# Kernel optimization log

Measured on AMD Instinct MI355X. Metric: run time of the kernel, lower is better.

Reference implementation:

```python
import jax, jax.numpy as jnp
import numpy as np

N_NODES = 50000
N_EDGES = 800000
N_GRAPHS = 512
D_IN, D_HID, D_EMB = 64, 128, 128


def _lin_params(key, d_in, d_out):
    kw, kb = jax.random.split(key)
    scale = 1.0 / np.sqrt(d_in)
    W = jax.random.uniform(kw, (d_in, d_out), minval=-scale, maxval=scale, dtype=jnp.float32)
    b = jax.random.uniform(kb, (d_out,), minval=-scale, maxval=scale, dtype=jnp.float32)
    return W, b


def setup_inputs() -> dict:
    key = jax.random.key(0)
    ks = jax.random.split(key, 12)
    x = jax.random.normal(ks[0], (N_NODES, D_IN), dtype=jnp.float32)
    edge_index = jax.random.randint(ks[1], (2, N_EDGES), 0, N_NODES, dtype=jnp.int64)
    batch = jnp.sort(jax.random.randint(ks[2], (N_NODES,), 0, N_GRAPHS, dtype=jnp.int64))
    Wq1, bq1 = _lin_params(ks[3], D_IN, D_HID)
    Wk1, bk1 = _lin_params(ks[4], D_IN, D_HID)
    Wv1, bv1 = _lin_params(ks[5], D_IN, D_HID)
    Ws1, bs1 = _lin_params(ks[6], D_IN, D_HID)
    Wq2, bq2 = _lin_params(ks[7], D_HID, D_EMB)
    Wk2, bk2 = _lin_params(ks[8], D_HID, D_EMB)
    Wv2, bv2 = _lin_params(ks[9], D_HID, D_EMB)
    Ws2, bs2 = _lin_params(ks[10], D_HID, D_EMB)
    return {
        'x': x, 'edge_index': edge_index, 'batch': batch,
        'Wq1': Wq1, 'bq1': bq1, 'Wk1': Wk1, 'bk1': bk1, 'Wv1': Wv1, 'bv1': bv1, 'Ws1': Ws1, 'bs1': bs1,
        'Wq2': Wq2, 'bq2': bq2, 'Wk2': Wk2, 'bk2': bk2, 'Wv2': Wv2, 'bv2': bv2, 'Ws2': Ws2, 'bs2': bs2,
    }


def _transformer_conv(x, src, dst, Wq, bq, Wk, bk, Wv, bv, Ws, bs):
    # PyG TransformerConv, heads=1, concat=True, root_weight=True, no edge_attr.
    d = Wq.shape[1]
    q = x @ Wq + bq          # [N, d]
    k = x @ Wk + bk
    v = x @ Wv + bv
    # per-edge attention score (gather at src/dst)
    score = jnp.sum(q[dst] * k[src], axis=-1) / jnp.sqrt(jnp.float32(d))  # [E]
    # segment softmax over destination neighborhoods
    m = jax.ops.segment_max(score, dst, num_segments=N_NODES)
    e = jnp.exp(score - m[dst])
    s = jax.ops.segment_sum(e, dst, num_segments=N_NODES)
    alpha = e / (s[dst] + 1e-16)  # [E]
    out = jax.ops.segment_sum(alpha[:, None] * v[src], dst, num_segments=N_NODES)  # [N, d]
    return out + (x @ Ws + bs)  # skip connection


def reference(x, edge_index, batch,
              Wq1, bq1, Wk1, bk1, Wv1, bv1, Ws1, bs1,
              Wq2, bq2, Wk2, bk2, Wv2, bv2, Ws2, bs2):
    src, dst = edge_index[0], edge_index[1]
    h = _transformer_conv(x, src, dst, Wq1, bq1, Wk1, bk1, Wv1, bv1, Ws1, bs1)
    h = jax.nn.relu(h)
    h = _transformer_conv(h, src, dst, Wq2, bq2, Wk2, bk2, Wv2, bv2, Ws2, bs2)
    # global mean pool over batch index
    sums = jax.ops.segment_sum(h, batch, num_segments=N_GRAPHS)
    counts = jax.ops.segment_sum(jnp.ones((h.shape[0],), dtype=h.dtype), batch, num_segments=N_GRAPHS)
    return sums / jnp.maximum(counts, 1.0)[:, None]
```

## Files before the change

kernel.cpp:

```cpp
#include <hip/hip_runtime.h>
#include <hip/hip_fp8.h>
#include <math.h>


constexpr int D1 = 64;
constexpr int DH = 128;
constexpr int SCHUNK = 1024;
constexpr float QSCALE2 = 0.12751743f;

typedef __attribute__((ext_vector_type(8))) short short8v;
typedef __attribute__((ext_vector_type(4))) float f32x4;
typedef __attribute__((ext_vector_type(2))) float f32x2;

#if __has_builtin(__builtin_amdgcn_cvt_pk_f32_fp8)
#define HW_FP8_DEC 1
#endif

__device__ inline unsigned short bf16r(float f) {
  unsigned u = __float_as_uint(f);
  return (unsigned short)((u + 0x7fffu + ((u >> 16) & 1u)) >> 16);
}

__device__ inline unsigned pack_bf16_2(float a, float b) {
  return (unsigned)bf16r(a) | ((unsigned)bf16r(b) << 16);
}

__device__ inline float bf16f(unsigned short u) {
  return __uint_as_float(((unsigned)u) << 16);
}

__device__ inline unsigned char fp8e(float f) {
  __hip_fp8_e4m3 h(f);
  return h.__x;
}

#ifndef HW_FP8_DEC
__device__ inline float fp8f_sw(unsigned b) {
  unsigned e = (b >> 3) & 15u, mm = b & 7u;
  float v;
  if (e == 0) v = (float)mm * 0.001953125f;
  else v = __uint_as_float(((e + 119u) << 23) | (mm << 20));
  return (b & 0x80u) ? -v : v;
}
#endif

__device__ inline void fp8_dec8(unsigned lo, unsigned hi, float* w) {
#ifdef HW_FP8_DEC
  f32x2 p01 = __builtin_amdgcn_cvt_pk_f32_fp8((int)lo, false);
  f32x2 p23 = __builtin_amdgcn_cvt_pk_f32_fp8((int)lo, true);
  f32x2 p45 = __builtin_amdgcn_cvt_pk_f32_fp8((int)hi, false);
  f32x2 p67 = __builtin_amdgcn_cvt_pk_f32_fp8((int)hi, true);
  w[0] = p01[0]; w[1] = p01[1]; w[2] = p23[0]; w[3] = p23[1];
  w[4] = p45[0]; w[5] = p45[1]; w[6] = p67[0]; w[7] = p67[1];
#else
  w[0] = fp8f_sw(lo & 0xffu); w[1] = fp8f_sw((lo >> 8) & 0xffu);
  w[2] = fp8f_sw((lo >> 16) & 0xffu); w[3] = fp8f_sw(lo >> 24);
  w[4] = fp8f_sw(hi & 0xffu); w[5] = fp8f_sw((hi >> 8) & 0xffu);
  w[6] = fp8f_sw((hi >> 16) & 0xffu); w[7] = fp8f_sw(hi >> 24);
#endif
}


__global__ __launch_bounds__(256) void hist_prep(
    const int* __restrict__ dst, int* __restrict__ deg, int* __restrict__ rank,
    int E, int nbHist,
    const float* w0, const float* w1, const float* w2, const float* w3,
    const float* w4, const float* w5, const float* w6, const float* w7,
    unsigned short* t0, unsigned short* t1, unsigned short* t2,
    unsigned short* t3, unsigned short* t4, unsigned short* t5,
    unsigned short* t6, unsigned short* t7,
    const float4* __restrict__ x, uint2* __restrict__ xb, int n4) {
  int b = blockIdx.x;
  int tid = threadIdx.x;
  if (b < nbHist) {
    int i = b * 256 + tid;
    if (i < (E >> 2)) {
      int4 d4 = ((const int4*)dst)[i];
      int4 r4;
      r4.x = atomicAdd(&deg[d4.x], 1);
      r4.y = atomicAdd(&deg[d4.y], 1);
      r4.z = atomicAdd(&deg[d4.z], 1);
      r4.w = atomicAdd(&deg[d4.w], 1);
      ((int4*)rank)[i] = r4;
    }
    if (b == 0 && tid == 0) {
      for (int e = E & ~3; e < E; ++e) rank[e] = atomicAdd(&deg[dst[e]], 1);
    }
    return;
  }
  int g = b - nbHist;
  if (g < 512) {
    int m = g >> 6, bx = g & 63;
    const float* W;
    unsigned short* T;
    switch (m) {
      case 0: W = w0; T = t0; break;
      case 1: W = w1; T = t1; break;
      case 2: W = w2; T = t2; break;
      case 3: W = w3; T = t3; break;
      case 4: W = w4; T = t4; break;
      case 5: W = w5; T = t5; break;
      case 6: W = w6; T = t6; break;
      default: W = w7; T = t7; break;
    }
    int din = (m < 4) ? 64 : 128;
    int total = din * 128;
    int i = bx * 256 + tid;
    if (i < total) {
      int r = i >> 7, c = i & 127;
      T[c * din + r] = bf16r(W[i]);
    }
    return;
  }
  int bx = g - 512;
  for (int i = bx * 256 + tid; i < n4; i += 256 * 256) {
    float4 v = x[i];
    uint2 o;
    o.x = pack_bf16_2(v.x, v.y);
    o.y = pack_bf16_2(v.z, v.w);
    xb[i] = o;
  }
}


__global__ void scan_chunks(const int* __restrict__ deg, int* __restrict__ incl,
                            int* __restrict__ sums, int N) {
  __shared__ int lds[256];
  int b = blockIdx.x, tid = threadIdx.x;
  int base = b * SCHUNK + tid * 4;
  int e0 = (base + 0 < N) ? deg[base + 0] : 0;
  int e1 = (base + 1 < N) ? deg[base + 1] : 0;
  int e2 = (base + 2 < N) ? deg[base + 2] : 0;
  int e3 = (base + 3 < N) ? deg[base + 3] : 0;
  int t0 = e0, t1 = t0 + e1, t2 = t1 + e2, t3 = t2 + e3;
  lds[tid] = t3;
  __syncthreads();
  for (int off = 1; off < 256; off <<= 1) {
    int v = (tid >= off) ? lds[tid - off] : 0;
    __syncthreads();
    lds[tid] += v;
    __syncthreads();
  }
  int excl = (tid > 0) ? lds[tid - 1] : 0;
  if (base + 0 < N) incl[base + 0] = t0 + excl;
  if (base + 1 < N) incl[base + 1] = t1 + excl;
  if (base + 2 < N) incl[base + 2] = t2 + excl;
  if (base + 3 < N) incl[base + 3] = t3 + excl;
  if (tid == 255) sums[b] = lds[255];
}

__global__ void finalize_rowptr(const int* __restrict__ incl, const int* __restrict__ sums,
                                int* __restrict__ rowptr, int N) {
  int n = blockIdx.x * blockDim.x + threadIdx.x;
  if (n < N) {
    int ch = n / SCHUNK;
    int off = 0;
    for (int i = 0; i < ch; ++i) off += sums[i];
    rowptr[n + 1] = incl[n] + off;
  }
  if (n == 0) rowptr[0] = 0;
}


template <int DIN>
__device__ __forceinline__ void gemm4_tile(
    int bx, int y, int tid,
    const unsigned short* __restrict__ xb, int N,
    const unsigned short* __restrict__ Wt0, const float* __restrict__ B0,
    const unsigned short* __restrict__ Wt1, const float* __restrict__ B1,
    const unsigned short* __restrict__ Wt2, const float* __restrict__ B2,
    const unsigned short* __restrict__ Wt3, const float* __restrict__ B3,
    unsigned short* __restrict__ Qb, unsigned char* __restrict__ KV,
    unsigned short* __restrict__ Os) {
  constexpr int DS = DIN + 8;
  __shared__ __align__(16) unsigned short As[128 * DS];
  __shared__ __align__(16) unsigned short Bs[128 * DS];
  const unsigned short* Wt;
  const float* Bias;
  switch (y) {
    case 0: Wt = Wt0; Bias = B0; break;
    case 1: Wt = Wt1; Bias = B1; break;
    case 2: Wt = Wt2; Bias = B2; break;
    default: Wt = Wt3; Bias = B3; break;
  }
  int n0 = bx * 128;

  constexpr int CPR = DIN / 8;
  constexpr int ACH = 128 * CPR;
#pragma unroll
  for (int c = tid; c < ACH; c += 512) {
    int row = c / CPR, c8 = c - row * CPR;
    int n = n0 + row;
    uint4 val = {0u, 0u, 0u, 0u};
    if (n < N) val = *(const uint4*)&xb[(size_t)n * DIN + c8 * 8];
    *(uint4*)&As[row * DS + c8 * 8] = val;
  }
#pragma unroll
  for (int c = tid; c < ACH; c += 512) {
    int row = c / CPR, c8 = c - row * CPR;
    uint4 val = *(const uint4*)&Wt[(size_t)row * DIN + c8 * 8];
    *(uint4*)&Bs[row * DS + c8 * 8] = val;
  }
  __syncthreads();

  int w = tid >> 6, lane = tid & 63, lr = lane & 15, lg = lane >> 4;
  int wr = w >> 2;
  int wc = w & 3;
  constexpr int KS = DIN / 32;

  short8v a[4][KS];
#pragma unroll
  for (int af = 0; af < 4; ++af)
#pragma unroll
    for (int ks = 0; ks < KS; ++ks)
      a[af][ks] = *(const short8v*)&As[(wr * 64 + af * 16 + lr) * DS + ks * 32 + lg * 8];

  f32x4 acc[4][2];
#pragma unroll
  for (int af = 0; af < 4; ++af)
#pragma unroll
    for (int nf = 0; nf < 2; ++nf) acc[af][nf] = (f32x4){0.f, 0.f, 0.f, 0.f};

#pragma unroll
  for (int ks = 0; ks < KS; ++ks) {
#pragma unroll
    for (int nf = 0; nf < 2; ++nf) {
      short8v b = *(const short8v*)&Bs[(wc * 32 + nf * 16 + lr) * DS + ks * 32 + lg * 8];
#pragma unroll
      for (int af = 0; af < 4; ++af)
        acc[af][nf] = __builtin_amdgcn_mfma_f32_16x16x32_bf16(a[af][ks], b, acc[af][nf], 0, 0, 0);
    }
  }

#pragma unroll
  for (int af = 0; af < 4; ++af) {
    int rbase = n0 + wr * 64 + af * 16 + lg * 4;
#pragma unroll
    for (int nf = 0; nf < 2; ++nf) {
      int col = wc * 32 + nf * 16 + lr;
      float bias = Bias[col];
      if (y == 0) {
#pragma unroll
        for (int r = 0; r < 4; ++r) {
          int n = rbase + r;
          if (n < N) Qb[(size_t)n * 128 + col] = bf16r((acc[af][nf][r] + bias) * QSCALE2);
        }
      } else if (y == 1) {
#pragma unroll
        for (int r = 0; r < 4; ++r) {
          int n = rbase + r;
          if (n < N) KV[(size_t)n * 256 + col] = fp8e(acc[af][nf][r] + bias);
        }
      } else if (y == 2) {
#pragma unroll
        for (int r = 0; r < 4; ++r) {
          int n = rbase + r;
          if (n < N) KV[(size_t)n * 256 + 128 + col] = fp8e(acc[af][nf][r] + bias);
        }
      } else {
#pragma unroll
        for (int r = 0; r < 4; ++r) {
          int n = rbase + r;
          if (n < N) Os[(size_t)n * 128 + col] = bf16r(acc[af][nf][r] + bias);
        }
      }
    }
  }
}


template <int DIN>
__global__ __launch_bounds__(512) void fill_gemm1(
    const int* __restrict__ src, const int* __restrict__ dst,
    const int* __restrict__ rank, const int* __restrict__ rowptr,
    int* __restrict__ csr_src, int E, int epb4,
    const unsigned short* __restrict__ xb, int N,
    const unsigned short* __restrict__ Wt0, const float* __restrict__ B0,
    const unsigned short* __restrict__ Wt1, const float* __restrict__ B1,
    const unsigned short* __restrict__ Wt2, const float* __restrict__ B2,
    const unsigned short* __restrict__ Wt3, const float* __restrict__ B3,
    unsigned short* __restrict__ Qb, unsigned char* __restrict__ KV,
    unsigned short* __restrict__ Os) {
  int b = blockIdx.x;
  int b5 = b / 5, r5 = b - b5 * 5;
  if (r5 == 0) {
    int e4 = E >> 2;
    int end = min((b5 + 1) * epb4, e4);
    for (int i = b5 * epb4 + threadIdx.x; i < end; i += 512) {
      int4 d4 = ((const int4*)dst)[i];
      int4 r4 = ((const int4*)rank)[i];
      int4 s4 = ((const int4*)src)[i];
      csr_src[rowptr[d4.x] + r4.x] = s4.x;
      csr_src[rowptr[d4.y] + r4.y] = s4.y;
      csr_src[rowptr[d4.z] + r4.z] = s4.z;
      csr_src[rowptr[d4.w] + r4.w] = s4.w;
    }
    if (b5 == 0 && threadIdx.x == 0) {
      for (int e = E & ~3; e < E; ++e) csr_src[rowptr[dst[e]] + rank[e]] = src[e];
    }
    return;
  }
  int g = b5 * 4 + r5 - 1;
  gemm4_tile<DIN>(g >> 2, g & 3, threadIdx.x, xb, N, Wt0, B0, Wt1, B1,
                  Wt2, B2, Wt3, B3, Qb, KV, Os);
}

template <int DIN>
__global__ __launch_bounds__(512) void gemm4(
    const unsigned short* __restrict__ xb, int N,
    const unsigned short* __restrict__ Wt0, const float* __restrict__ B0,
    const unsigned short* __restrict__ Wt1, const float* __restrict__ B1,
    const unsigned short* __restrict__ Wt2, const float* __restrict__ B2,
    const unsigned short* __restrict__ Wt3, const float* __restrict__ B3,
    unsigned short* __restrict__ Qb, unsigned char* __restrict__ KV,
    unsigned short* __restrict__ Os) {
  gemm4_tile<DIN>(blockIdx.x, blockIdx.y, threadIdx.x, xb, N, Wt0, B0, Wt1, B1,
                  Wt2, B2, Wt3, B3, Qb, KV, Os);
}


template <bool RELU>
__global__ __launch_bounds__(256) void edge_agg4(
    const unsigned short* __restrict__ qb, const unsigned char* __restrict__ kv,
    const int* __restrict__ rowptr, const int* __restrict__ csr_src,
    const unsigned short* __restrict__ skipb, unsigned short* __restrict__ outp,
    int N) {
  int tid = threadIdx.x;
  int lane = tid & 63;
  int wv = tid >> 6;
  int n = blockIdx.x * 4 + wv;
  if (n >= N) return;
  int g4 = lane >> 4;
  int sl = lane & 15;
  uint4 qp = *(const uint4*)&qb[(size_t)n * 128 + 8 * sl];
  float q0 = bf16f((unsigned short)(qp.x & 0xffff)), q1 = bf16f((unsigned short)(qp.x >> 16));
  float q2 = bf16f((unsigned short)(qp.y & 0xffff)), q3 = bf16f((unsigned short)(qp.y >> 16));
  float q4 = bf16f((unsigned short)(qp.z & 0xffff)), q5 = bf16f((unsigned short)(qp.z >> 16));
  float q6 = bf16f((unsigned short)(qp.w & 0xffff)), q7 = bf16f((unsigned short)(qp.w >> 16));
  int beg = rowptr[n];
  int deg = rowptr[n + 1] - beg;
  float m = -1e30f, lsum = 0.f;
  float acc[8];
#pragma unroll
  for (int j = 0; j < 8; ++j) acc[j] = 0.f;
  int cnt = (deg - g4 + 3) >> 2;
  if (cnt < 0) cnt = 0;
  const int* cp = csr_src + beg + g4;
  unsigned ko = 8u * sl, vo = 128u + 8u * sl;
  uint2 k0 = {0, 0}, k1 = {0, 0};
  uint2 v0 = {0, 0}, v1 = {0, 0};
  if (cnt >= 1) {
    unsigned r = (unsigned)cp[0] * 256u;
    k0 = *(const uint2*)(kv + r + ko);
    v0 = *(const uint2*)(kv + r + vo);
  }
  if (cnt >= 2) {
    unsigned r = (unsigned)cp[4] * 256u;
    k1 = *(const uint2*)(kv + r + ko);
    v1 = *(const uint2*)(kv + r + vo);
  }
  for (int it = 0; it < cnt; ++it) {
    uint2 kc = k0;
    uint2 vc = v0;
    k0 = k1;
    v0 = v1;
    if (it + 2 < cnt) {
      unsigned r = (unsigned)cp[4 * (it + 2)] * 256u;
      k1 = *(const uint2*)(kv + r + ko);
      v1 = *(const uint2*)(kv + r + vo);
    }
    float kd[8];
    fp8_dec8(kc.x, kc.y, kd);
    float d = q0 * kd[0] + q1 * kd[1] + q2 * kd[2] + q3 * kd[3] +
              q4 * kd[4] + q5 * kd[5] + q6 * kd[6] + q7 * kd[7];
#pragma unroll
    for (int off = 1; off < 16; off <<= 1) d += __shfl_xor(d, off);
    float w[8];
    fp8_dec8(vc.x, vc.y, w);
    if (d > m + 8.f) {
      float cf = exp2f(m - d);
      lsum = lsum * cf + 1.f;
#pragma unroll
      for (int j = 0; j < 8; ++j) acc[j] = acc[j] * cf + w[j];
      m = d;
    } else {
      float ef = exp2f(d - m);
      lsum += ef;
#pragma unroll
      for (int j = 0; j < 8; ++j) acc[j] += ef * w[j];
    }
  }
#pragma unroll
  for (int ofs = 16; ofs <= 32; ofs <<= 1) {
    float mo = __shfl_xor(m, ofs);
    float lo = __shfl_xor(lsum, ofs);
    float ao[8];
#pragma unroll
    for (int j = 0; j < 8; ++j) ao[j] = __shfl_xor(acc[j], ofs);
    float M = fmaxf(m, mo);
    float c1 = exp2f(m - M);
    float c2 = exp2f(mo - M);
    lsum = lsum * c1 + lo * c2;
#pragma unroll
    for (int j = 0; j < 8; ++j) acc[j] = acc[j] * c1 + ao[j] * c2;
    m = M;
  }
  if (lane < 16) {
    float rl = (deg > 0) ? 1.f / (lsum + 1e-16f) : 0.f;
    uint4 sp = *(const uint4*)&skipb[(size_t)n * 128 + 8 * sl];
    float o0 = bf16f((unsigned short)(sp.x & 0xffff)) + acc[0] * rl;
    float o1 = bf16f((unsigned short)(sp.x >> 16)) + acc[1] * rl;
    float o2 = bf16f((unsigned short)(sp.y & 0xffff)) + acc[2] * rl;
    float o3 = bf16f((unsigned short)(sp.y >> 16)) + acc[3] * rl;
    float o4 = bf16f((unsigned short)(sp.z & 0xffff)) + acc[4] * rl;
    float o5 = bf16f((unsigned short)(sp.z >> 16)) + acc[5] * rl;
    float o6 = bf16f((unsigned short)(sp.w & 0xffff)) + acc[6] * rl;
    float o7 = bf16f((unsigned short)(sp.w >> 16)) + acc[7] * rl;
    if (RELU) {
      o0 = fmaxf(o0, 0.f); o1 = fmaxf(o1, 0.f); o2 = fmaxf(o2, 0.f); o3 = fmaxf(o3, 0.f);
      o4 = fmaxf(o4, 0.f); o5 = fmaxf(o5, 0.f); o6 = fmaxf(o6, 0.f); o7 = fmaxf(o7, 0.f);
    }
    uint4 pk;
    pk.x = pack_bf16_2(o0, o1);
    pk.y = pack_bf16_2(o2, o3);
    pk.z = pack_bf16_2(o4, o5);
    pk.w = pack_bf16_2(o6, o7);
    *(uint4*)&outp[(size_t)n * 128 + 8 * sl] = pk;
  }
}


__global__ __launch_bounds__(128) void pool_kernel(const unsigned short* __restrict__ h,
                                                   const int* __restrict__ batch,
                                                   float* __restrict__ out, int N) {
  int g = blockIdx.x;
  int lo = 0, hi = N;
  while (lo < hi) { int mid = (lo + hi) >> 1; if (batch[mid] < g) lo = mid + 1; else hi = mid; }
  int s0 = lo;
  hi = N;
  while (lo < hi) { int mid = (lo + hi) >> 1; if (batch[mid] <= g) lo = mid + 1; else hi = mid; }
  int s1 = lo;
  int j = threadIdx.x;
  float acc = 0.f;
  for (int n = s0; n < s1; ++n) acc += bf16f(h[(size_t)n * 128 + j]);
  out[(size_t)g * 128 + j] = acc / fmaxf((float)(s1 - s0), 1.f);
}


extern "C" void kernel_launch(void* const* d_in, const int* in_sizes, int n_in,
                              void* d_out, int out_size, void* d_ws, size_t ws_size,
                              hipStream_t stream) {
  const float* x = (const float*)d_in[0];
  const int* ei = (const int*)d_in[1];
  const int* batch = (const int*)d_in[2];
  const float* Wq1 = (const float*)d_in[3];
  const float* bq1 = (const float*)d_in[4];
  const float* Wk1 = (const float*)d_in[5];
  const float* bk1 = (const float*)d_in[6];
  const float* Wv1 = (const float*)d_in[7];
  const float* bv1 = (const float*)d_in[8];
  const float* Ws1 = (const float*)d_in[9];
  const float* bs1 = (const float*)d_in[10];
  const float* Wq2 = (const float*)d_in[11];
  const float* bq2 = (const float*)d_in[12];
  const float* Wk2 = (const float*)d_in[13];
  const float* bk2 = (const float*)d_in[14];
  const float* Wv2 = (const float*)d_in[15];
  const float* bv2 = (const float*)d_in[16];
  const float* Ws2 = (const float*)d_in[17];
  const float* bs2 = (const float*)d_in[18];

  int N = in_sizes[0] / D1;
  int E = in_sizes[1] / 2;
  int NG = out_size / DH;
  const int* src = ei;
  const int* dst = ei + E;

  char* ws = (char*)d_ws;
  unsigned short* qb = (unsigned short*)ws;  ws += (size_t)N * DH * 2;
  unsigned char* kvb = (unsigned char*)ws;   ws += (size_t)N * 256;
  ws = (char*)(((size_t)ws + 255) & ~(size_t)255);
  unsigned short* sb = (unsigned short*)ws;  ws += (size_t)N * DH * 2;
  unsigned short* h1b = (unsigned short*)ws; ws += (size_t)N * DH * 2;
  unsigned short* xb = (unsigned short*)ws;  ws += (size_t)N * D1 * 2;
  unsigned short* wt[8];
  for (int m = 0; m < 8; ++m) {
    int din = (m < 4) ? 64 : 128;
    wt[m] = (unsigned short*)ws;
    ws += (size_t)128 * din * 2;
  }
  ws = (char*)(((size_t)ws + 255) & ~(size_t)255);
  int* rowptr = (int*)ws; ws += (size_t)(N + 1) * 4;
  ws = (char*)(((size_t)ws + 255) & ~(size_t)255);
  int* deg = (int*)ws;  ws += (size_t)N * 4;
  int* incl = (int*)ws; ws += (size_t)N * 4;
  int* sums = (int*)ws; ws += 1024;
  int* rank = (int*)ws; ws += (size_t)E * 4;
  int* csr = (int*)ws;  ws += (size_t)E * 4;

  int nch = (N + SCHUNK - 1) / SCHUNK;
  int nbHist = ((E >> 2) + 255) / 256;
  int nb = (N + 127) / 128;
  int epb4 = ((E >> 2) + nb - 1) / nb;

  hipMemsetAsync(deg, 0, (size_t)N * 4, stream);

  hist_prep<<<nbHist + 768, 256, 0, stream>>>(
      dst, deg, rank, E, nbHist, Wq1, Wk1, Wv1, Ws1, Wq2, Wk2, Wv2, Ws2,
      wt[0], wt[1], wt[2], wt[3], wt[4], wt[5], wt[6], wt[7],
      (const float4*)x, (uint2*)xb, N * D1 / 4);
  scan_chunks<<<nch, 256, 0, stream>>>(deg, incl, sums, N);
  finalize_rowptr<<<(N + 255) / 256, 256, 0, stream>>>(incl, sums, rowptr, N);
  fill_gemm1<D1><<<nb * 5, 512, 0, stream>>>(
      src, dst, rank, rowptr, csr, E, epb4, xb, N,
      wt[0], bq1, wt[1], bk1, wt[2], bv1, wt[3], bs1, qb, kvb, sb);
  edge_agg4<true><<<(N + 3) / 4, 256, 0, stream>>>(
      qb, kvb, rowptr, csr, sb, h1b, N);
  gemm4<DH><<<dim3(nb, 4), 512, 0, stream>>>(h1b, N, wt[4], bq2, wt[5], bk2,
                                             wt[6], bv2, wt[7], bs2, qb, kvb, sb);
  edge_agg4<false><<<(N + 3) / 4, 256, 0, stream>>>(
      qb, kvb, rowptr, csr, sb, h1b, N);
  pool_kernel<<<NG, 128, 0, stream>>>(h1b, batch, (float*)d_out, N);
}
```

Baseline: 239.7 us.

## Process eight edges per wave with 16-byte loads and packed float2 math

The edge aggregation kernel now splits each 64-lane wave into 8 groups of 8 lanes, each lane handling 16 features, instead of 4 groups of 16 lanes with 8 features. Loads of K/V rows become 16-byte vectors, and the dot product and accumulation use float2 vector types so the compiler can emit packed FMA instructions. The goal is more edges in flight per wave and fewer shuffles per edge. In exchange each lane holds more registers, and there is one extra cross-group merge step with more shuffles at the end.

```diff
diff --git a/kernel.cpp b/kernel.cpp
--- a/kernel.cpp
+++ b/kernel.cpp
@@ -27,6 +27,13 @@
 
 __device__ inline float bf16f(unsigned short u) {
   return __uint_as_float(((unsigned)u) << 16);
+}
+
+__device__ inline f32x2 bf16_2f(unsigned u) {
+  f32x2 r;
+  r[0] = __uint_as_float(u << 16);
+  r[1] = __uint_as_float(u & 0xffff0000u);
+  return r;
 }
 
 __device__ inline unsigned char fp8e(float f) {
@@ -44,19 +51,15 @@
 }
 #endif
 
-__device__ inline void fp8_dec8(unsigned lo, unsigned hi, float* w) {
+__device__ inline void fp8_dec4(unsigned w, f32x2* lo, f32x2* hi) {
 #ifdef HW_FP8_DEC
-  f32x2 p01 = __builtin_amdgcn_cvt_pk_f32_fp8((int)lo, false);
-  f32x2 p23 = __builtin_amdgcn_cvt_pk_f32_fp8((int)lo, true);
-  f32x2 p45 = __builtin_amdgcn_cvt_pk_f32_fp8((int)hi, false);
-  f32x2 p67 = __builtin_amdgcn_cvt_pk_f32_fp8((int)hi, true);
-  w[0] = p01[0]; w[1] = p01[1]; w[2] = p23[0]; w[3] = p23[1];
-  w[4] = p45[0]; w[5] = p45[1]; w[6] = p67[0]; w[7] = p67[1];
+  *lo = __builtin_amdgcn_cvt_pk_f32_fp8((int)w, false);
+  *hi = __builtin_amdgcn_cvt_pk_f32_fp8((int)w, true);
 #else
-  w[0] = fp8f_sw(lo & 0xffu); w[1] = fp8f_sw((lo >> 8) & 0xffu);
-  w[2] = fp8f_sw((lo >> 16) & 0xffu); w[3] = fp8f_sw(lo >> 24);
-  w[4] = fp8f_sw(hi & 0xffu); w[5] = fp8f_sw((hi >> 8) & 0xffu);
-  w[6] = fp8f_sw((hi >> 16) & 0xffu); w[7] = fp8f_sw(hi >> 24);
+  (*lo)[0] = fp8f_sw(w & 0xffu);
+  (*lo)[1] = fp8f_sw((w >> 8) & 0xffu);
+  (*hi)[0] = fp8f_sw((w >> 16) & 0xffu);
+  (*hi)[1] = fp8f_sw(w >> 24);
 #endif
 }
 
@@ -320,7 +323,7 @@
 
 
 template <bool RELU>
-__global__ __launch_bounds__(256) void edge_agg4(
+__global__ __launch_bounds__(256) void edge_agg8(
     const unsigned short* __restrict__ qb, const unsigned char* __restrict__ kv,
     const int* __restrict__ rowptr, const int* __restrict__ csr_src,
     const unsigned short* __restrict__ skipb, unsigned short* __restrict__ outp,
@@ -330,102 +333,117 @@
   int wv = tid >> 6;
   int n = blockIdx.x * 4 + wv;
   if (n >= N) return;
-  int g4 = lane >> 4;
-  int sl = lane & 15;
-  uint4 qp = *(const uint4*)&qb[(size_t)n * 128 + 8 * sl];
-  float q0 = bf16f((unsigned short)(qp.x & 0xffff)), q1 = bf16f((unsigned short)(qp.x >> 16));
-  float q2 = bf16f((unsigned short)(qp.y & 0xffff)), q3 = bf16f((unsigned short)(qp.y >> 16));
-  float q4 = bf16f((unsigned short)(qp.z & 0xffff)), q5 = bf16f((unsigned short)(qp.z >> 16));
-  float q6 = bf16f((unsigned short)(qp.w & 0xffff)), q7 = bf16f((unsigned short)(qp.w >> 16));
+  int g8 = lane >> 3;
+  int sl = lane & 7;
+  uint4 qa = *(const uint4*)&qb[(size_t)n * 128 + 16 * sl];
+  uint4 qc = *(const uint4*)&qb[(size_t)n * 128 + 16 * sl + 8];
+  f32x2 q2[8];
+  q2[0] = bf16_2f(qa.x); q2[1] = bf16_2f(qa.y);
+  q2[2] = bf16_2f(qa.z); q2[3] = bf16_2f(qa.w);
+  q2[4] = bf16_2f(qc.x); q2[5] = bf16_2f(qc.y);
+  q2[6] = bf16_2f(qc.z); q2[7] = bf16_2f(qc.w);
   int beg = rowptr[n];
   int deg = rowptr[n + 1] - beg;
   float m = -1e30f, lsum = 0.f;
-  float acc[8];
-#pragma unroll
-  for (int j = 0; j < 8; ++j) acc[j] = 0.f;
-  int cnt = (deg - g4 + 3) >> 2;
-  if (cnt < 0) cnt = 0;
-  const int* cp = csr_src + beg + g4;
-  unsigned ko = 8u * sl, vo = 128u + 8u * sl;
-  uint2 k0 = {0, 0}, k1 = {0, 0};
-  uint2 v0 = {0, 0}, v1 = {0, 0};
+  f32x2 acc2[8];
+#pragma unroll
+  for (int j = 0; j < 8; ++j) acc2[j] = (f32x2){0.f, 0.f};
+  int cnt = (deg - g8 + 7) >> 3;
+  const int* cp = csr_src + beg + g8;
+  unsigned ko = 16u * sl, vo = 128u + 16u * sl;
+  uint4 k0 = {0, 0, 0, 0}, k1 = {0, 0, 0, 0};
+  uint4 v0 = {0, 0, 0, 0}, v1 = {0, 0, 0, 0};
   if (cnt >= 1) {
     unsigned r = (unsigned)cp[0] * 256u;
-    k0 = *(const uint2*)(kv + r + ko);
-    v0 = *(const uint2*)(kv + r + vo);
+    k0 = *(const uint4*)(kv + r + ko);
+    v0 = *(const uint4*)(kv + r + vo);
   }
   if (cnt >= 2) {
-    unsigned r = (unsigned)cp[4] * 256u;
-    k1 = *(const uint2*)(kv + r + ko);
-    v1 = *(const uint2*)(kv + r + vo);
+    unsigned r = (unsigned)cp[8] * 256u;
+    k1 = *(const uint4*)(kv + r + ko);
+    v1 = *(const uint4*)(kv + r + vo);
   }
   for (int it = 0; it < cnt; ++it) {
-    uint2 kc = k0;
-    uint2 vc = v0;
+    uint4 kc = k0;
+    uint4 vc = v0;
     k0 = k1;
     v0 = v1;
     if (it + 2 < cnt) {
-      unsigned r = (unsigned)cp[4 * (it + 2)] * 256u;
-      k1 = *(const uint2*)(kv + r + ko);
-      v1 = *(const uint2*)(kv + r + vo);
-    }
-    float kd[8];
-    fp8_dec8(kc.x, kc.y, kd);
-    float d = q0 * kd[0] + q1 * kd[1] + q2 * kd[2] + q3 * kd[3] +
-              q4 * kd[4] + q5 * kd[5] + q6 * kd[6] + q7 * kd[7];
-#pragma unroll
-    for (int off = 1; off < 16; off <<= 1) d += __shfl_xor(d, off);
-    float w[8];
-    fp8_dec8(vc.x, vc.y, w);
+      unsigned r = (unsigned)cp[8 * (it + 2)] * 256u;
+      k1 = *(const uint4*)(kv + r + ko);
+      v1 = *(const uint4*)(kv + r + vo);
+    }
+    f32x2 kd[8];
+    fp8_dec4(kc.x, &kd[0], &kd[1]);
+    fp8_dec4(kc.y, &kd[2], &kd[3]);
+    fp8_dec4(kc.z, &kd[4], &kd[5]);
+    fp8_dec4(kc.w, &kd[6], &kd[7]);
+    f32x2 d2 = q2[0] * kd[0];
+#pragma unroll
+    for (int j = 1; j < 8; ++j) d2 += q2[j] * kd[j];
+    float d = d2[0] + d2[1];
+#pragma unroll
+    for (int off = 1; off < 8; off <<= 1) d += __shfl_xor(d, off);
+    f32x2 w2[8];
+    fp8_dec4(vc.x, &w2[0], &w2[1]);
+    fp8_dec4(vc.y, &w2[2], &w2[3]);
+    fp8_dec4(vc.z, &w2[4], &w2[5]);
+    fp8_dec4(vc.w, &w2[6], &w2[7]);
     if (d > m + 8.f) {
       float cf = exp2f(m - d);
+      f32x2 cf2 = {cf, cf};
       lsum = lsum * cf + 1.f;
 #pragma unroll
-      for (int j = 0; j < 8; ++j) acc[j] = acc[j] * cf + w[j];
+      for (int j = 0; j < 8; ++j) acc2[j] = acc2[j] * cf2 + w2[j];
       m = d;
     } else {
       float ef = exp2f(d - m);
+      f32x2 ef2 = {ef, ef};
       lsum += ef;
 #pragma unroll
-      for (int j = 0; j < 8; ++j) acc[j] += ef * w[j];
-    }
-  }
-#pragma unroll
-  for (int ofs = 16; ofs <= 32; ofs <<= 1) {
+      for (int j = 0; j < 8; ++j) acc2[j] += ef2 * w2[j];
+    }
+  }
+#pragma unroll
+  for (int ofs = 8; ofs <= 32; ofs <<= 1) {
     float mo = __shfl_xor(m, ofs);
     float lo = __shfl_xor(lsum, ofs);
-    float ao[8];
-#pragma unroll
-    for (int j = 0; j < 8; ++j) ao[j] = __shfl_xor(acc[j], ofs);
+    f32x2 ao[8];
+#pragma unroll
+    for (int j = 0; j < 8; ++j) {
+      ao[j][0] = __shfl_xor(acc2[j][0], ofs);
+      ao[j][1] = __shfl_xor(acc2[j][1], ofs);
+    }
     float M = fmaxf(m, mo);
     float c1 = exp2f(m - M);
     float c2 = exp2f(mo - M);
+    f32x2 c12 = {c1, c1}, c22 = {c2, c2};
     lsum = lsum * c1 + lo * c2;
 #pragma unroll
-    for (int j = 0; j < 8; ++j) acc[j] = acc[j] * c1 + ao[j] * c2;
+    for (int j = 0; j < 8; ++j) acc2[j] = acc2[j] * c12 + ao[j] * c22;
     m = M;
   }
-  if (lane < 16) {
+  if (lane < 8) {
     float rl = (deg > 0) ? 1.f / (lsum + 1e-16f) : 0.f;
-    uint4 sp = *(const uint4*)&skipb[(size_t)n * 128 + 8 * sl];
-    float o0 = bf16f((unsigned short)(sp.x & 0xffff)) + acc[0] * rl;
-    float o1 = bf16f((unsigned short)(sp.x >> 16)) + acc[1] * rl;
-    float o2 = bf16f((unsigned short)(sp.y & 0xffff)) + acc[2] * rl;
-    float o3 = bf16f((unsigned short)(sp.y >> 16)) + acc[3] * rl;
-    float o4 = bf16f((unsigned short)(sp.z & 0xffff)) + acc[4] * rl;
-    float o5 = bf16f((unsigned short)(sp.z >> 16)) + acc[5] * rl;
-    float o6 = bf16f((unsigned short)(sp.w & 0xffff)) + acc[6] * rl;
-    float o7 = bf16f((unsigned short)(sp.w >> 16)) + acc[7] * rl;
-    if (RELU) {
-      o0 = fmaxf(o0, 0.f); o1 = fmaxf(o1, 0.f); o2 = fmaxf(o2, 0.f); o3 = fmaxf(o3, 0.f);
-      o4 = fmaxf(o4, 0.f); o5 = fmaxf(o5, 0.f); o6 = fmaxf(o6, 0.f); o7 = fmaxf(o7, 0.f);
-    }
-    uint4 pk;
-    pk.x = pack_bf16_2(o0, o1);
-    pk.y = pack_bf16_2(o2, o3);
-    pk.z = pack_bf16_2(o4, o5);
-    pk.w = pack_bf16_2(o6, o7);
-    *(uint4*)&outp[(size_t)n * 128 + 8 * sl] = pk;
+    uint4 sa = *(const uint4*)&skipb[(size_t)n * 128 + 16 * sl];
+    uint4 sc = *(const uint4*)&skipb[(size_t)n * 128 + 16 * sl + 8];
+    unsigned sw[8] = {sa.x, sa.y, sa.z, sa.w, sc.x, sc.y, sc.z, sc.w};
+    unsigned ow[8];
+#pragma unroll
+    for (int j = 0; j < 8; ++j) {
+      f32x2 s2 = bf16_2f(sw[j]);
+      float oa = s2[0] + acc2[j][0] * rl;
+      float ob = s2[1] + acc2[j][1] * rl;
+      if (RELU) {
+        oa = fmaxf(oa, 0.f);
+        ob = fmaxf(ob, 0.f);
+      }
+      ow[j] = pack_bf16_2(oa, ob);
+    }
+    uint4 p0 = {ow[0], ow[1], ow[2], ow[3]};
+    uint4 p1 = {ow[4], ow[5], ow[6], ow[7]};
+    *(uint4*)&outp[(size_t)n * 128 + 16 * sl] = p0;
+    *(uint4*)&outp[(size_t)n * 128 + 16 * sl + 8] = p1;
   }
 }
 
@@ -514,11 +532,11 @@
   fill_gemm1<D1><<<nb * 5, 512, 0, stream>>>(
       src, dst, rank, rowptr, csr, E, epb4, xb, N,
       wt[0], bq1, wt[1], bk1, wt[2], bv1, wt[3], bs1, qb, kvb, sb);
-  edge_agg4<true><<<(N + 3) / 4, 256, 0, stream>>>(
+  edge_agg8<true><<<(N + 3) / 4, 256, 0, stream>>>(
       qb, kvb, rowptr, csr, sb, h1b, N);
   gemm4<DH><<<dim3(nb, 4), 512, 0, stream>>>(h1b, N, wt[4], bq2, wt[5], bk2,
                                              wt[6], bv2, wt[7], bs2, qb, kvb, sb);
-  edge_agg4<false><<<(N + 3) / 4, 256, 0, stream>>>(
+  edge_agg8<false><<<(N + 3) / 4, 256, 0, stream>>>(
       qb, kvb, rowptr, csr, sb, h1b, N);
   pool_kernel<<<NG, 128, 0, stream>>>(h1b, batch, (float*)d_out, N);
 }
```

Result: slower. 259.9 us (+8.4%).
